# Optimization experiments

Measured on AMD Instinct MI355X. Metric: run time of the kernel, lower is better.

## Reference

```python
import jax, jax.numpy as jnp
import numpy as np

N, E, D, H, G = 50000, 1_600_000, 13, 32, 128
EPS = 1e-5


def _lin(k, fan_in, fan_out):
    kw, kb = jax.random.split(k)
    bound = 1.0 / np.sqrt(fan_in)
    W = jax.random.uniform(kw, (fan_in, fan_out), jnp.float32, -bound, bound)
    b = jax.random.uniform(kb, (fan_out,), jnp.float32, -bound, bound)
    return W, b


def setup_inputs() -> dict:
    key = jax.random.key(0)
    ks = jax.random.split(key, 10)
    x = jax.random.normal(ks[0], (N, D), jnp.float32)
    edge_index = jax.random.randint(ks[1], (2, E), 0, N)
    batch = jnp.sort(jax.random.randint(ks[2], (N,), 0, G))
    bn_gamma = jnp.ones((D,), jnp.float32)
    bn_beta = jnp.zeros((D,), jnp.float32)
    in_w1, in_b1 = _lin(ks[3], D, H)
    in_w2, in_b2 = _lin(ks[4], H, H)
    conv_w1, conv_b1 = _lin(ks[5], 2 * (H + D), 2 * H)
    conv_w2, conv_b2 = _lin(ks[6], 2 * H, H)
    out_w1, out_b1 = _lin(ks[7], H + D, H)
    out_w2, out_b2 = _lin(ks[8], H, 1)
    return dict(x=x, edge_index=edge_index, batch=batch,
                bn_gamma=bn_gamma, bn_beta=bn_beta,
                in_w1=in_w1, in_b1=in_b1, in_w2=in_w2, in_b2=in_b2,
                conv_w1=conv_w1, conv_b1=conv_b1, conv_w2=conv_w2, conv_b2=conv_b2,
                out_w1=out_w1, out_b1=out_b1, out_w2=out_w2, out_b2=out_b2)


def reference(x, edge_index, batch, bn_gamma, bn_beta,
              in_w1, in_b1, in_w2, in_b2,
              conv_w1, conv_b1, conv_w2, conv_b2,
              out_w1, out_b1, out_w2, out_b2):
    # BatchNorm1d (training-mode batch statistics, biased variance)
    mu = jnp.mean(x, axis=0)
    var = jnp.mean((x - mu) ** 2, axis=0)
    X = (x - mu) / jnp.sqrt(var + EPS) * bn_gamma + bn_beta  # [N, D]
    # inputnet
    Hn = jnp.tanh(jax.nn.relu(X @ in_w1 + in_b1) @ in_w2 + in_b2)  # [N, H]
    feat = jnp.concatenate([Hn, X], axis=-1)  # [N, H+D]
    # n_iters = 1 EdgeConv iteration: message = nn([x_i, x_j - x_i]), aggr='add' at target i
    src, dst = edge_index[0], edge_index[1]
    x_i = feat[dst]                               # [E, H+D] target
    x_j = feat[src]                               # [E, H+D] source
    m = jnp.concatenate([x_i, x_j - x_i], axis=-1)  # [E, 2(H+D)]
    m = jnp.tanh(jax.nn.relu(m @ conv_w1 + conv_b1) @ conv_w2 + conv_b2)  # [E, H]
    Hn = jax.ops.segment_sum(m, dst, num_segments=N)  # [N, H]
    feat = jnp.concatenate([Hn, X], axis=-1)  # [N, H+D]
    # global_mean_pool over graphs
    sums = jax.ops.segment_sum(feat, batch, num_segments=G)  # [G, H+D]
    counts = jax.ops.segment_sum(jnp.ones((feat.shape[0], 1), feat.dtype), batch, num_segments=G)
    x_mean = sums / jnp.maximum(counts, 1.0)
    # outputnet
    return jax.nn.sigmoid(jax.nn.relu(x_mean @ out_w1 + out_b1) @ out_w2 + out_b2)  # [G, 1]
```

## Files before the change

### kernel.cpp

```cpp
#include <hip/hip_runtime.h>


typedef __attribute__((ext_vector_type(4))) float floatx4;
typedef __attribute__((ext_vector_type(8))) short short8;
typedef __attribute__((ext_vector_type(8))) _Float16 half8;
typedef __attribute__((ext_vector_type(2))) __fp16 fp16x2;

__device__ __forceinline__ unsigned short f2bf(float f) {
    unsigned int u = __float_as_uint(f);
    u += 0x7FFFu + ((u >> 16) & 1u);
    return (unsigned short)(u >> 16);
}
__device__ __forceinline__ unsigned short f2h(float f) {
    _Float16 h = (_Float16)f;
    return __builtin_bit_cast(unsigned short, h);
}
__device__ __forceinline__ float h2f(unsigned short u) {
    return (float)__builtin_bit_cast(_Float16, u);
}
__device__ __forceinline__ float fast_tanh(float x) {
    float ax = fminf(fabsf(x), 20.0f);
    float e = __expf(2.0f * ax);
    float r = 1.0f - 2.0f * __builtin_amdgcn_rcpf(e + 1.0f);
    return copysignf(r, x);
}
__device__ __forceinline__ float fast_sigmoid(float x) {
    float xc = fminf(fmaxf(x, -30.f), 30.f);
    return 1.0f / (1.0f + __expf(-xc));
}
__device__ __forceinline__ unsigned int pk_h2(float a, float b) {
    fp16x2 p = __builtin_amdgcn_cvt_pkrtz(a, b);
    return __builtin_bit_cast(unsigned int, p);
}
__device__ __forceinline__ void atomic_pk_add_f16(unsigned short* addr, unsigned int packed) {
    asm volatile("global_atomic_pk_add_f16 %0, %1, off" :: "v"(addr), "v"(packed) : "memory");
}

#define NBLK_STAT 120

__global__ __launch_bounds__(256) void k_bnstat(const float* __restrict__ x, int N,
                                                float* __restrict__ part,
                                                uint4* __restrict__ HnZ, int hnq,
                                                float* __restrict__ gacc, int gn) {
    int tid = blockIdx.x * blockDim.x + threadIdx.x;
    int stride = gridDim.x * blockDim.x;
    uint4 z4 = make_uint4(0u, 0u, 0u, 0u);
    for (int i = tid; i < hnq; i += stride) HnZ[i] = z4;
    for (int i = tid; i < gn; i += stride) gacc[i] = 0.f;

    float s[13], q[13];
#pragma unroll
    for (int d = 0; d < 13; d++) { s[d] = 0.f; q[d] = 0.f; }
    for (int n = tid; n < N; n += stride) {
        const float* row = x + (size_t)n * 13;
#pragma unroll
        for (int d = 0; d < 13; d++) { float f = row[d]; s[d] += f; q[d] += f * f; }
    }
#pragma unroll
    for (int d = 0; d < 13; d++) {
        for (int off = 32; off > 0; off >>= 1) {
            s[d] += __shfl_down(s[d], off, 64);
            q[d] += __shfl_down(q[d], off, 64);
        }
    }
    __shared__ float red[4][26];
    int w = threadIdx.x >> 6;
    if ((threadIdx.x & 63) == 0) {
#pragma unroll
        for (int d = 0; d < 13; d++) { red[w][d] = s[d]; red[w][13 + d] = q[d]; }
    }
    __syncthreads();
    if (threadIdx.x < 26) {
        float v = red[0][threadIdx.x] + red[1][threadIdx.x] + red[2][threadIdx.x] + red[3][threadIdx.x];
        int d = threadIdx.x;
        if (d < 13) part[blockIdx.x * 32 + d] = v;
        else        part[NBLK_STAT * 32 + blockIdx.x * 32 + (d - 13)] = v;
    }
}

#define FP 72
#define WP 72
__global__ __launch_bounds__(128) void k_node(
    const float* __restrict__ x, const int* __restrict__ batch,
    const float* __restrict__ bn_g, const float* __restrict__ bn_b,
    const float* __restrict__ in_w1, const float* __restrict__ in_b1,
    const float* __restrict__ in_w2, const float* __restrict__ in_b2,
    const float* __restrict__ conv_w1, const float* __restrict__ conv_b1,
    const float* __restrict__ part,
    unsigned short* __restrict__ A, unsigned short* __restrict__ Bm,
    float* __restrict__ gacc, int N) {
    __shared__ float sW1[13 * 32], sB1[32], sW2[32 * 32], sB2[32];
    __shared__ float sScl[16], sShf[16];
    __shared__ unsigned short sWcatT[128 * WP];
    __shared__ unsigned short sFeat[128 * FP];
    int tid = threadIdx.x;

    for (int i = tid; i < 13 * 32; i += 128) sW1[i] = in_w1[i];
    if (tid < 32) { sB1[tid] = in_b1[tid]; sB2[tid] = in_b2[tid]; }
    for (int i = tid; i < 32 * 32; i += 128) sW2[i] = in_w2[i];
    for (int i = tid; i < 128 * 64; i += 128) {
        int c = i >> 6, k = i & 63;
        float v = 0.f;
        if (k < 45) {
            int cc = c & 63;
            float bot = conv_w1[(45 + k) * 64 + cc];
            v = (c < 64) ? (conv_w1[k * 64 + cc] - bot) : bot;
        }
        sWcatT[c * WP + k] = f2bf(v);
    }
    if (tid < 13) {
        float su = 0.f, sq = 0.f;
        for (int b = 0; b < NBLK_STAT; b++) {
            su += part[b * 32 + tid];
            sq += part[NBLK_STAT * 32 + b * 32 + tid];
        }
        float invN = 1.0f / (float)N;
        float mu = su * invN;
        float var = fmaxf(sq * invN - mu * mu, 0.f);
        float sc = bn_g[tid] / sqrtf(var + 1e-5f);
        sScl[tid] = sc;
        sShf[tid] = bn_b[tid] - mu * sc;
    }
    __syncthreads();

    int n = blockIdx.x * 128 + tid;
    bool valid = (n < N);
    int nl = valid ? n : (N - 1);

    float X[13];
#pragma unroll
    for (int d = 0; d < 13; d++)
        X[d] = x[(size_t)nl * 13 + d] * sScl[d] + sShf[d];
    float h1[32];
#pragma unroll
    for (int j = 0; j < 32; j++) {
        float acc = sB1[j];
#pragma unroll
        for (int d = 0; d < 13; d++) acc += X[d] * sW1[d * 32 + j];
        h1[j] = fmaxf(acc, 0.f);
    }
    float h2[32];
#pragma unroll
    for (int j = 0; j < 32; j++) {
        float acc = sB2[j];
#pragma unroll
        for (int k = 0; k < 32; k++) acc += h1[k] * sW2[k * 32 + j];
        h2[j] = fast_tanh(acc);
    }

    unsigned int fw[16];
#pragma unroll
    for (int i = 0; i < 16; i++) fw[i] = 0;
    if (valid) {
#pragma unroll
        for (int i = 0; i < 16; i++)
            fw[i] = (unsigned)f2bf(h2[2 * i]) | ((unsigned)f2bf(h2[2 * i + 1]) << 16);
    }
    unsigned int xw[7];
#pragma unroll
    for (int i = 0; i < 7; i++) xw[i] = 0;
    if (valid) {
#pragma unroll
        for (int i = 0; i < 6; i++)
            xw[i] = (unsigned)f2bf(X[2 * i]) | ((unsigned)f2bf(X[2 * i + 1]) << 16);
        xw[6] = (unsigned)f2bf(X[12]);
    }
    {
        unsigned short* row = sFeat + tid * FP;
        ((uint4*)row)[0] = make_uint4(fw[0], fw[1], fw[2], fw[3]);
        ((uint4*)row)[1] = make_uint4(fw[4], fw[5], fw[6], fw[7]);
        ((uint4*)row)[2] = make_uint4(fw[8], fw[9], fw[10], fw[11]);
        ((uint4*)row)[3] = make_uint4(fw[12], fw[13], fw[14], fw[15]);
        ((uint4*)row)[4] = make_uint4(xw[0], xw[1], xw[2], xw[3]);
        ((uint4*)row)[5] = make_uint4(xw[4], xw[5], xw[6], 0u);
        ((uint4*)row)[6] = make_uint4(0u, 0u, 0u, 0u);
        ((uint4*)row)[7] = make_uint4(0u, 0u, 0u, 0u);
    }

    {
        int g = valid ? batch[n] : -1;
        unsigned long long uni = __ballot(g == __shfl(g, 0, 64));
        if (uni == ~0ull && g >= 0) {
            float red[14];
#pragma unroll
            for (int d = 0; d < 13; d++) red[d] = X[d];
            red[13] = 1.0f;
#pragma unroll
            for (int d = 0; d < 14; d++)
                for (int off = 32; off > 0; off >>= 1)
                    red[d] += __shfl_down(red[d], off, 64);
            if ((tid & 63) == 0) {
#pragma unroll
                for (int d = 0; d < 13; d++) unsafeAtomicAdd(&gacc[g * 46 + 32 + d], red[d]);
                unsafeAtomicAdd(&gacc[g * 46 + 45], red[13]);
            }
        } else if (valid) {
#pragma unroll
            for (int d = 0; d < 13; d++) unsafeAtomicAdd(&gacc[g * 46 + 32 + d], X[d]);
            unsafeAtomicAdd(&gacc[g * 46 + 45], 1.0f);
        }
    }
    __syncthreads();

    int lane = tid & 63;
    int w = tid >> 6;
    int q = lane >> 4;
    int m = lane & 15;

    short8 wf[2][8];
#pragma unroll
    for (int ks = 0; ks < 2; ks++)
#pragma unroll
        for (int t = 0; t < 8; t++) {
            wf[ks][t] = *(const short8*)(sWcatT + (t * 16 + m) * WP + ks * 32 + q * 8);
        }
    float cb1v[4];
#pragma unroll
    for (int t = 0; t < 4; t++) cb1v[t] = conv_b1[t * 16 + m];

    int base = blockIdx.x * 128 + w * 64;
#pragma unroll
    for (int tile = 0; tile < 4; tile++) {
        const unsigned short* ar = sFeat + (w * 64 + tile * 16 + m) * FP;
        short8 a0 = *(const short8*)(ar + q * 8);
        short8 a1 = *(const short8*)(ar + 32 + q * 8);
        floatx4 c[8];
#pragma unroll
        for (int t = 0; t < 8; t++) {
            floatx4 z = {0.f, 0.f, 0.f, 0.f};
            c[t] = __builtin_amdgcn_mfma_f32_16x16x32_bf16(a0, wf[0][t], z, 0, 0, 0);
            c[t] = __builtin_amdgcn_mfma_f32_16x16x32_bf16(a1, wf[1][t], c[t], 0, 0, 0);
        }
#pragma unroll
        for (int r = 0; r < 4; r++) {
            int row = base + tile * 16 + (q << 2) + r;
            if (row < N) {
#pragma unroll
                for (int t = 0; t < 4; t++)
                    A[(size_t)row * 64 + t * 16 + m] = f2h(c[t][r] + cb1v[t]);
#pragma unroll
                for (int t = 4; t < 8; t++)
                    Bm[(size_t)row * 64 + (t - 4) * 16 + m] = f2h(c[t][r]);
            }
        }
    }
}

__global__ __launch_bounds__(256) void k_edge(
    const int* __restrict__ ei,
    const unsigned short* __restrict__ A, const unsigned short* __restrict__ Bm,
    const float* __restrict__ conv_w2, const float* __restrict__ conv_b2,
    unsigned short* __restrict__ Hn, int E) {
    int lane = threadIdx.x & 63;
    int wid  = blockIdx.x * (blockDim.x >> 6) + (threadIdx.x >> 6);
    int nw   = gridDim.x * (blockDim.x >> 6);
    int q = lane >> 4;
    int m = lane & 15;

    half8 wf[2][2];
#pragma unroll
    for (int s = 0; s < 2; s++)
#pragma unroll
        for (int t = 0; t < 2; t++)
#pragma unroll
            for (int j = 0; j < 8; j++)
                wf[s][t][j] = (_Float16)conv_w2[(s * 32 + q * 8 + j) * 32 + 2 * m + t];
    float cb2a = conv_b2[2 * m];
    float cb2b = conv_b2[2 * m + 1];

    const int* srcp = ei;
    const int* dstp = ei + E;
    int npairs = E >> 5;

    const half8 zero8 = (half8)(_Float16)0.0f;

    for (int p = wid; p < npairs; p += nw) {
        int e0 = p << 5;
        int vd0 = dstp[e0 + m];
        int vs0 = srcp[e0 + m];
        int vd1 = dstp[e0 + 16 + m];
        int vs1 = srcp[e0 + 16 + m];
        uint4 av0a = *(const uint4*)(A  + (size_t)vd0 * 64 + q * 8);
        uint4 av0b = *(const uint4*)(A  + (size_t)vd0 * 64 + 32 + q * 8);
        uint4 bv0a = *(const uint4*)(Bm + (size_t)vs0 * 64 + q * 8);
        uint4 bv0b = *(const uint4*)(Bm + (size_t)vs0 * 64 + 32 + q * 8);
        uint4 av1a = *(const uint4*)(A  + (size_t)vd1 * 64 + q * 8);
        uint4 av1b = *(const uint4*)(A  + (size_t)vd1 * 64 + 32 + q * 8);
        uint4 bv1a = *(const uint4*)(Bm + (size_t)vs1 * 64 + q * 8);
        uint4 bv1b = *(const uint4*)(Bm + (size_t)vs1 * 64 + 32 + q * 8);

        floatx4 c00 = {0.f, 0.f, 0.f, 0.f}, c01 = {0.f, 0.f, 0.f, 0.f};
        floatx4 c10 = {0.f, 0.f, 0.f, 0.f}, c11 = {0.f, 0.f, 0.f, 0.f};

        auto mk = [&zero8](uint4 av, uint4 bv) -> half8 {
            half8 a = __builtin_bit_cast(half8, av);
            half8 b = __builtin_bit_cast(half8, bv);
            half8 s = a + b;
            return __builtin_elementwise_max(s, zero8);
        };
        half8 h0a = mk(av0a, bv0a);
        half8 h0b = mk(av0b, bv0b);
        half8 h1a = mk(av1a, bv1a);
        half8 h1b = mk(av1b, bv1b);

        c00 = __builtin_amdgcn_mfma_f32_16x16x32_f16(h0a, wf[0][0], c00, 0, 0, 0);
        c01 = __builtin_amdgcn_mfma_f32_16x16x32_f16(h0a, wf[0][1], c01, 0, 0, 0);
        c10 = __builtin_amdgcn_mfma_f32_16x16x32_f16(h1a, wf[0][0], c10, 0, 0, 0);
        c11 = __builtin_amdgcn_mfma_f32_16x16x32_f16(h1a, wf[0][1], c11, 0, 0, 0);
        c00 = __builtin_amdgcn_mfma_f32_16x16x32_f16(h0b, wf[1][0], c00, 0, 0, 0);
        c01 = __builtin_amdgcn_mfma_f32_16x16x32_f16(h0b, wf[1][1], c01, 0, 0, 0);
        c10 = __builtin_amdgcn_mfma_f32_16x16x32_f16(h1b, wf[1][0], c10, 0, 0, 0);
        c11 = __builtin_amdgcn_mfma_f32_16x16x32_f16(h1b, wf[1][1], c11, 0, 0, 0);

#pragma unroll
        for (int r = 0; r < 4; r++) {
            int m2 = (q << 2) + r;
            int dd0 = __shfl(vd0, m2, 64);
            int dd1 = __shfl(vd1, m2, 64);
            float o00 = fast_tanh(c00[r] + cb2a);
            float o01 = fast_tanh(c01[r] + cb2b);
            float o10 = fast_tanh(c10[r] + cb2a);
            float o11 = fast_tanh(c11[r] + cb2b);
            atomic_pk_add_f16(Hn + (size_t)dd0 * 32 + 2 * m, pk_h2(o00, o01));
            atomic_pk_add_f16(Hn + (size_t)dd1 * 32 + 2 * m, pk_h2(o10, o11));
        }
    }

    int tstart = npairs << 5;
    int tail = E - tstart;
    if (tail && wid == 0 && lane < tail) {
        int e = tstart + lane;
        int vd = dstp[e], vs = srcp[e];
        float h[64];
        for (int k = 0; k < 64; k++) {
            float a = h2f(A[(size_t)vd * 64 + k]);
            float b = h2f(Bm[(size_t)vs * 64 + k]);
            h[k] = fmaxf(a + b, 0.f);
        }
        for (int j = 0; j < 16; j++) {
            float acc0 = conv_b2[2 * j], acc1 = conv_b2[2 * j + 1];
            for (int k = 0; k < 64; k++) {
                acc0 += h[k] * conv_w2[k * 32 + 2 * j];
                acc1 += h[k] * conv_w2[k * 32 + 2 * j + 1];
            }
            atomic_pk_add_f16(Hn + (size_t)vd * 32 + 2 * j, pk_h2(fast_tanh(acc0), fast_tanh(acc1)));
        }
    }
}

__global__ __launch_bounds__(256) void k_pool(const unsigned short* __restrict__ Hn,
                                              const int* __restrict__ batch,
                                              float* __restrict__ gacc, int N) {
    const int NPB = 512;
    int c = threadIdx.x & 31;
    int r = threadIdx.x >> 5;
    int n0 = blockIdx.x * NPB;
    int nend = min(n0 + NPB, N);
    int gcur = -1;
    float acc = 0.f;
    for (int n = n0 + r; n < nend; n += 8) {
        int g = batch[n];
        if (g != gcur) {
            if (gcur >= 0) unsafeAtomicAdd(&gacc[gcur * 46 + c], acc);
            gcur = g; acc = 0.f;
        }
        acc += h2f(Hn[(size_t)n * 32 + c]);
    }
    if (gcur >= 0) unsafeAtomicAdd(&gacc[gcur * 46 + c], acc);
}

__global__ void k_out(const float* __restrict__ gacc,
                      const float* __restrict__ out_w1, const float* __restrict__ out_b1,
                      const float* __restrict__ out_w2, const float* __restrict__ out_b2,
                      float* __restrict__ out, int G) {
    int g = blockIdx.x * blockDim.x + threadIdx.x;
    if (g >= G) return;
    float cnt = fmaxf(gacc[g * 46 + 45], 1.0f);
    float inv = 1.0f / cnt;
    float f[45];
#pragma unroll
    for (int i = 0; i < 45; i++) f[i] = gacc[g * 46 + i] * inv;
    float h[32];
#pragma unroll
    for (int j = 0; j < 32; j++) {
        float acc = out_b1[j];
#pragma unroll
        for (int k = 0; k < 45; k++) acc += f[k] * out_w1[k * 32 + j];
        h[j] = fmaxf(acc, 0.f);
    }
    float o = out_b2[0];
#pragma unroll
    for (int j = 0; j < 32; j++) o += h[j] * out_w2[j];
    out[g] = fast_sigmoid(o);
}

extern "C" void kernel_launch(void* const* d_in, const int* in_sizes, int n_in,
                              void* d_out, int out_size, void* d_ws, size_t ws_size,
                              hipStream_t stream) {
    const float* x      = (const float*)d_in[0];
    const int*   ei     = (const int*)d_in[1];
    const int*   batch  = (const int*)d_in[2];
    const float* bn_g   = (const float*)d_in[3];
    const float* bn_b   = (const float*)d_in[4];
    const float* in_w1  = (const float*)d_in[5];
    const float* in_b1  = (const float*)d_in[6];
    const float* in_w2  = (const float*)d_in[7];
    const float* in_b2  = (const float*)d_in[8];
    const float* cw1    = (const float*)d_in[9];
    const float* cb1    = (const float*)d_in[10];
    const float* cw2    = (const float*)d_in[11];
    const float* cb2    = (const float*)d_in[12];
    const float* ow1    = (const float*)d_in[13];
    const float* ob1    = (const float*)d_in[14];
    const float* ow2    = (const float*)d_in[15];
    const float* ob2    = (const float*)d_in[16];

    int N = in_sizes[0] / 13;
    int E = in_sizes[1] / 2;
    int G = out_size;
    int Npad = (N + 255) & ~255;

    auto al = [](size_t v) { return (v + 255) & ~(size_t)255; };
    char* ws = (char*)d_ws;
    size_t hn_off   = 0;
    size_t gacc_off = al((size_t)N * 32 * 2);
    size_t part_off = gacc_off + al((size_t)G * 46 * 4);
    size_t a_off    = part_off + al(2 * NBLK_STAT * 32 * 4);
    size_t b_off    = a_off + al((size_t)Npad * 64 * 2);

    unsigned short* Hn = (unsigned short*)(ws + hn_off);
    float* gacc = (float*)(ws + gacc_off);
    float* part = (float*)(ws + part_off);
    unsigned short* A  = (unsigned short*)(ws + a_off);
    unsigned short* Bm = (unsigned short*)(ws + b_off);

    int hnq = (N * 32 * 2) / 16;
    int gn  = G * 46;

    k_bnstat<<<NBLK_STAT, 256, 0, stream>>>(x, N, part, (uint4*)Hn, hnq, gacc, gn);
    k_node<<<(N + 127) / 128, 128, 0, stream>>>(x, batch, bn_g, bn_b,
                                                in_w1, in_b1, in_w2, in_b2,
                                                cw1, cb1, part, A, Bm, gacc, N);
    k_edge<<<2048, 256, 0, stream>>>(ei, A, Bm, cw2, cb2, Hn, E);
    k_pool<<<(N + 511) / 512, 256, 0, stream>>>(Hn, batch, gacc, N);
    k_out<<<1, 128, 0, stream>>>(gacc, ow1, ob1, ow2, ob2, (float*)d_out, G);
}
```

Before: 285.9 us.

## Build CSR by destination and replace atomic edge scatter with per-node gather

```diff
diff --git a/kernel.cpp b/kernel.cpp
--- a/kernel.cpp
+++ b/kernel.cpp
@@ -32,21 +32,17 @@
     fp16x2 p = __builtin_amdgcn_cvt_pkrtz(a, b);
     return __builtin_bit_cast(unsigned int, p);
 }
-__device__ __forceinline__ void atomic_pk_add_f16(unsigned short* addr, unsigned int packed) {
-    asm volatile("global_atomic_pk_add_f16 %0, %1, off" :: "v"(addr), "v"(packed) : "memory");
-}
 
 #define NBLK_STAT 120
 
 __global__ __launch_bounds__(256) void k_bnstat(const float* __restrict__ x, int N,
                                                 float* __restrict__ part,
-                                                uint4* __restrict__ HnZ, int hnq,
-                                                float* __restrict__ gacc, int gn) {
+                                                float* __restrict__ gacc, int gn,
+                                                int* __restrict__ cnt, int cn) {
     int tid = blockIdx.x * blockDim.x + threadIdx.x;
     int stride = gridDim.x * blockDim.x;
-    uint4 z4 = make_uint4(0u, 0u, 0u, 0u);
-    for (int i = tid; i < hnq; i += stride) HnZ[i] = z4;
     for (int i = tid; i < gn; i += stride) gacc[i] = 0.f;
+    for (int i = tid; i < cn; i += stride) cnt[i] = 0;
 
     float s[13], q[13];
 #pragma unroll
@@ -75,6 +71,68 @@
         int d = threadIdx.x;
         if (d < 13) part[blockIdx.x * 32 + d] = v;
         else        part[NBLK_STAT * 32 + blockIdx.x * 32 + (d - 13)] = v;
+    }
+}
+
+__global__ __launch_bounds__(256) void k_hist(const int* __restrict__ ei,
+                                              int* __restrict__ cnt, int E) {
+    const int* dstp = ei + E;
+    int tid = blockIdx.x * blockDim.x + threadIdx.x;
+    int stride = gridDim.x * blockDim.x;
+    for (int e = tid; e < E; e += stride) atomicAdd(&cnt[dstp[e]], 1);
+}
+
+__global__ __launch_bounds__(1024) void k_scan1(int* __restrict__ cnt,
+                                                int* __restrict__ bsum, int N) {
+    __shared__ int sd[1024];
+    int t = threadIdx.x;
+    int i = blockIdx.x * 1024 + t;
+    int v = (i < N) ? cnt[i] : 0;
+    sd[t] = v;
+    __syncthreads();
+    for (int off = 1; off < 1024; off <<= 1) {
+        int a = (t >= off) ? sd[t - off] : 0;
+        __syncthreads();
+        sd[t] += a;
+        __syncthreads();
+    }
+    if (i < N) cnt[i] = sd[t] - v;
+    if (t == 1023) bsum[blockIdx.x] = sd[1023];
+}
+
+__global__ __launch_bounds__(256) void k_fill(const int* __restrict__ cnt,
+                                              const int* __restrict__ bsum,
+                                              int* __restrict__ cursor, int N, int nb) {
+    __shared__ int sboff[64];
+    int t = threadIdx.x;
+    if (t < 64) {
+        int v = (t < nb) ? bsum[t] : 0;
+        for (int off = 1; off < 64; off <<= 1) {
+            int u = __shfl_up(v, off, 64);
+            if (t >= off) v += u;
+        }
+        sboff[t] = v;
+    }
+    __syncthreads();
+    int i = blockIdx.x * blockDim.x + t;
+    if (i < N) {
+        int blk = i >> 10;
+        int boff = (blk == 0) ? 0 : sboff[blk - 1];
+        cursor[i] = cnt[i] + boff;
+    }
+}
+
+__global__ __launch_bounds__(256) void k_scatter(const int* __restrict__ ei,
+                                                 int* __restrict__ cursor,
+                                                 int* __restrict__ ssorted, int E) {
+    const int* srcp = ei;
+    const int* dstp = ei + E;
+    int tid = blockIdx.x * blockDim.x + threadIdx.x;
+    int stride = gridDim.x * blockDim.x;
+    for (int e = tid; e < E; e += stride) {
+        int d = dstp[e];
+        int pos = atomicAdd(&cursor[d], 1);
+        ssorted[pos] = srcp[e];
     }
 }
 
@@ -246,11 +304,12 @@
     }
 }
 
-__global__ __launch_bounds__(256) void k_edge(
-    const int* __restrict__ ei,
+__global__ __launch_bounds__(256) void k_edge2(
+    const int* __restrict__ cursor,
+    const int* __restrict__ ssorted,
     const unsigned short* __restrict__ A, const unsigned short* __restrict__ Bm,
     const float* __restrict__ conv_w2, const float* __restrict__ conv_b2,
-    unsigned short* __restrict__ Hn, int E) {
+    unsigned short* __restrict__ Hn, int N) {
     int lane = threadIdx.x & 63;
     int wid  = blockIdx.x * (blockDim.x >> 6) + (threadIdx.x >> 6);
     int nw   = gridDim.x * (blockDim.x >> 6);
@@ -268,83 +327,64 @@
     float cb2a = conv_b2[2 * m];
     float cb2b = conv_b2[2 * m + 1];
 
-    const int* srcp = ei;
-    const int* dstp = ei + E;
-    int npairs = E >> 5;
-
     const half8 zero8 = (half8)(_Float16)0.0f;
 
-    for (int p = wid; p < npairs; p += nw) {
-        int e0 = p << 5;
-        int vd0 = dstp[e0 + m];
-        int vs0 = srcp[e0 + m];
-        int vd1 = dstp[e0 + 16 + m];
-        int vs1 = srcp[e0 + 16 + m];
-        uint4 av0a = *(const uint4*)(A  + (size_t)vd0 * 64 + q * 8);
-        uint4 av0b = *(const uint4*)(A  + (size_t)vd0 * 64 + 32 + q * 8);
-        uint4 bv0a = *(const uint4*)(Bm + (size_t)vs0 * 64 + q * 8);
-        uint4 bv0b = *(const uint4*)(Bm + (size_t)vs0 * 64 + 32 + q * 8);
-        uint4 av1a = *(const uint4*)(A  + (size_t)vd1 * 64 + q * 8);
-        uint4 av1b = *(const uint4*)(A  + (size_t)vd1 * 64 + 32 + q * 8);
-        uint4 bv1a = *(const uint4*)(Bm + (size_t)vs1 * 64 + q * 8);
-        uint4 bv1b = *(const uint4*)(Bm + (size_t)vs1 * 64 + 32 + q * 8);
-
-        floatx4 c00 = {0.f, 0.f, 0.f, 0.f}, c01 = {0.f, 0.f, 0.f, 0.f};
-        floatx4 c10 = {0.f, 0.f, 0.f, 0.f}, c11 = {0.f, 0.f, 0.f, 0.f};
-
-        auto mk = [&zero8](uint4 av, uint4 bv) -> half8 {
-            half8 a = __builtin_bit_cast(half8, av);
-            half8 b = __builtin_bit_cast(half8, bv);
-            half8 s = a + b;
-            return __builtin_elementwise_max(s, zero8);
-        };
-        half8 h0a = mk(av0a, bv0a);
-        half8 h0b = mk(av0b, bv0b);
-        half8 h1a = mk(av1a, bv1a);
-        half8 h1b = mk(av1b, bv1b);
-
-        c00 = __builtin_amdgcn_mfma_f32_16x16x32_f16(h0a, wf[0][0], c00, 0, 0, 0);
-        c01 = __builtin_amdgcn_mfma_f32_16x16x32_f16(h0a, wf[0][1], c01, 0, 0, 0);
-        c10 = __builtin_amdgcn_mfma_f32_16x16x32_f16(h1a, wf[0][0], c10, 0, 0, 0);
-        c11 = __builtin_amdgcn_mfma_f32_16x16x32_f16(h1a, wf[0][1], c11, 0, 0, 0);
-        c00 = __builtin_amdgcn_mfma_f32_16x16x32_f16(h0b, wf[1][0], c00, 0, 0, 0);
-        c01 = __builtin_amdgcn_mfma_f32_16x16x32_f16(h0b, wf[1][1], c01, 0, 0, 0);
-        c10 = __builtin_amdgcn_mfma_f32_16x16x32_f16(h1b, wf[1][0], c10, 0, 0, 0);
-        c11 = __builtin_amdgcn_mfma_f32_16x16x32_f16(h1b, wf[1][1], c11, 0, 0, 0);
-
-#pragma unroll
-        for (int r = 0; r < 4; r++) {
-            int m2 = (q << 2) + r;
-            int dd0 = __shfl(vd0, m2, 64);
-            int dd1 = __shfl(vd1, m2, 64);
-            float o00 = fast_tanh(c00[r] + cb2a);
-            float o01 = fast_tanh(c01[r] + cb2b);
-            float o10 = fast_tanh(c10[r] + cb2a);
-            float o11 = fast_tanh(c11[r] + cb2b);
-            atomic_pk_add_f16(Hn + (size_t)dd0 * 32 + 2 * m, pk_h2(o00, o01));
-            atomic_pk_add_f16(Hn + (size_t)dd1 * 32 + 2 * m, pk_h2(o10, o11));
-        }
-    }
-
-    int tstart = npairs << 5;
-    int tail = E - tstart;
-    if (tail && wid == 0 && lane < tail) {
-        int e = tstart + lane;
-        int vd = dstp[e], vs = srcp[e];
-        float h[64];
-        for (int k = 0; k < 64; k++) {
-            float a = h2f(A[(size_t)vd * 64 + k]);
-            float b = h2f(Bm[(size_t)vs * 64 + k]);
-            h[k] = fmaxf(a + b, 0.f);
-        }
-        for (int j = 0; j < 16; j++) {
-            float acc0 = conv_b2[2 * j], acc1 = conv_b2[2 * j + 1];
-            for (int k = 0; k < 64; k++) {
-                acc0 += h[k] * conv_w2[k * 32 + 2 * j];
-                acc1 += h[k] * conv_w2[k * 32 + 2 * j + 1];
+    for (int d = wid; d < N; d += nw) {
+        int end = cursor[d];
+        int beg = (d == 0) ? 0 : cursor[d - 1];
+        int deg = end - beg;
+
+        half8 af0 = __builtin_bit_cast(half8, *(const uint4*)(A + (size_t)d * 64 + q * 8));
+        half8 af1 = __builtin_bit_cast(half8, *(const uint4*)(A + (size_t)d * 64 + 32 + q * 8));
+
+        float acc0 = 0.f, acc1 = 0.f;
+        for (int c = 0; c < deg; c += 32) {
+            int lim = end - 1;
+            int i0 = beg + c + m;
+            int s0 = ssorted[min(i0, lim)];
+            int s1 = ssorted[min(i0 + 16, lim)];
+            uint4 b0a = *(const uint4*)(Bm + (size_t)s0 * 64 + q * 8);
+            uint4 b0b = *(const uint4*)(Bm + (size_t)s0 * 64 + 32 + q * 8);
+            uint4 b1a = *(const uint4*)(Bm + (size_t)s1 * 64 + q * 8);
+            uint4 b1b = *(const uint4*)(Bm + (size_t)s1 * 64 + 32 + q * 8);
+
+            half8 h0a = __builtin_elementwise_max(af0 + __builtin_bit_cast(half8, b0a), zero8);
+            half8 h0b = __builtin_elementwise_max(af1 + __builtin_bit_cast(half8, b0b), zero8);
+            half8 h1a = __builtin_elementwise_max(af0 + __builtin_bit_cast(half8, b1a), zero8);
+            half8 h1b = __builtin_elementwise_max(af1 + __builtin_bit_cast(half8, b1b), zero8);
+
+            floatx4 c00 = {0.f, 0.f, 0.f, 0.f}, c01 = {0.f, 0.f, 0.f, 0.f};
+            floatx4 c10 = {0.f, 0.f, 0.f, 0.f}, c11 = {0.f, 0.f, 0.f, 0.f};
+            c00 = __builtin_amdgcn_mfma_f32_16x16x32_f16(h0a, wf[0][0], c00, 0, 0, 0);
+            c01 = __builtin_amdgcn_mfma_f32_16x16x32_f16(h0a, wf[0][1], c01, 0, 0, 0);
+            c10 = __builtin_amdgcn_mfma_f32_16x16x32_f16(h1a, wf[0][0], c10, 0, 0, 0);
+            c11 = __builtin_amdgcn_mfma_f32_16x16x32_f16(h1a, wf[0][1], c11, 0, 0, 0);
+            c00 = __builtin_amdgcn_mfma_f32_16x16x32_f16(h0b, wf[1][0], c00, 0, 0, 0);
+            c01 = __builtin_amdgcn_mfma_f32_16x16x32_f16(h0b, wf[1][1], c01, 0, 0, 0);
+            c10 = __builtin_amdgcn_mfma_f32_16x16x32_f16(h1b, wf[1][0], c10, 0, 0, 0);
+            c11 = __builtin_amdgcn_mfma_f32_16x16x32_f16(h1b, wf[1][1], c11, 0, 0, 0);
+
+            int j = q << 2;
+#pragma unroll
+            for (int r = 0; r < 4; r++) {
+                bool v0 = (c + j + r) < deg;
+                bool v1 = (c + 16 + j + r) < deg;
+                float t00 = fast_tanh(c00[r] + cb2a);
+                float t01 = fast_tanh(c01[r] + cb2b);
+                float t10 = fast_tanh(c10[r] + cb2a);
+                float t11 = fast_tanh(c11[r] + cb2b);
+                acc0 += v0 ? t00 : 0.f;
+                acc1 += v0 ? t01 : 0.f;
+                acc0 += v1 ? t10 : 0.f;
+                acc1 += v1 ? t11 : 0.f;
             }
-            atomic_pk_add_f16(Hn + (size_t)vd * 32 + 2 * j, pk_h2(fast_tanh(acc0), fast_tanh(acc1)));
-        }
+        }
+        acc0 += __shfl_xor(acc0, 16, 64);
+        acc0 += __shfl_xor(acc0, 32, 64);
+        acc1 += __shfl_xor(acc1, 16, 64);
+        acc1 += __shfl_xor(acc1, 32, 64);
+        if (q == 0)
+            *(unsigned int*)(Hn + (size_t)d * 32 + 2 * m) = pk_h2(acc0, acc1);
     }
 }
 
@@ -427,21 +467,33 @@
     size_t part_off = gacc_off + al((size_t)G * 46 * 4);
     size_t a_off    = part_off + al(2 * NBLK_STAT * 32 * 4);
     size_t b_off    = a_off + al((size_t)Npad * 64 * 2);
+    size_t cnt_off  = b_off + al((size_t)Npad * 64 * 2);
+    size_t bsum_off = cnt_off + al((size_t)N * 4);
+    size_t cur_off  = bsum_off + al(64 * 4);
+    size_t srt_off  = cur_off + al((size_t)N * 4);
 
     unsigned short* Hn = (unsigned short*)(ws + hn_off);
     float* gacc = (float*)(ws + gacc_off);
     float* part = (float*)(ws + part_off);
     unsigned short* A  = (unsigned short*)(ws + a_off);
     unsigned short* Bm = (unsigned short*)(ws + b_off);
-
-    int hnq = (N * 32 * 2) / 16;
+    int* cnt     = (int*)(ws + cnt_off);
+    int* bsum    = (int*)(ws + bsum_off);
+    int* cursor  = (int*)(ws + cur_off);
+    int* ssorted = (int*)(ws + srt_off);
+
     int gn  = G * 46;
-
-    k_bnstat<<<NBLK_STAT, 256, 0, stream>>>(x, N, part, (uint4*)Hn, hnq, gacc, gn);
+    int nb1 = (N + 1023) >> 10;
+
+    k_bnstat<<<NBLK_STAT, 256, 0, stream>>>(x, N, part, gacc, gn, cnt, N);
+    k_hist<<<512, 256, 0, stream>>>(ei, cnt, E);
+    k_scan1<<<nb1, 1024, 0, stream>>>(cnt, bsum, N);
+    k_fill<<<(N + 255) / 256, 256, 0, stream>>>(cnt, bsum, cursor, N, nb1);
+    k_scatter<<<1024, 256, 0, stream>>>(ei, cursor, ssorted, E);
     k_node<<<(N + 127) / 128, 128, 0, stream>>>(x, batch, bn_g, bn_b,
                                                 in_w1, in_b1, in_w2, in_b2,
                                                 cw1, cb1, part, A, Bm, gacc, N);
-    k_edge<<<2048, 256, 0, stream>>>(ei, A, Bm, cw2, cb2, Hn, E);
+    k_edge2<<<2048, 256, 0, stream>>>(cursor, ssorted, A, Bm, cw2, cb2, Hn, N);
     k_pool<<<(N + 511) / 512, 256, 0, stream>>>(Hn, batch, gacc, N);
     k_out<<<1, 128, 0, stream>>>(gacc, ow1, ob1, ow2, ob2, (float*)d_out, G);
 }
```

Measured after the change: 464.0 us. +62.3%, slower.

## Fuse edge, pool and output kernels into one cooperative kernel with grid syncs

Applied to the files above, without the earlier changes.

```diff
diff --git a/kernel.cpp b/kernel.cpp
--- a/kernel.cpp
+++ b/kernel.cpp
@@ -1,10 +1,13 @@
 #include <hip/hip_runtime.h>
+#include <hip/hip_cooperative_groups.h>
 
 
 typedef __attribute__((ext_vector_type(4))) float floatx4;
 typedef __attribute__((ext_vector_type(8))) short short8;
 typedef __attribute__((ext_vector_type(8))) _Float16 half8;
 typedef __attribute__((ext_vector_type(2))) __fp16 fp16x2;
+
+namespace cg = cooperative_groups;
 
 __device__ __forceinline__ unsigned short f2bf(float f) {
     unsigned int u = __float_as_uint(f);
@@ -91,6 +94,7 @@
     float* __restrict__ gacc, int N) {
     __shared__ float sW1[13 * 32], sB1[32], sW2[32 * 32], sB2[32];
     __shared__ float sScl[16], sShf[16];
+    __shared__ float sRedS[13][8], sRedQ[13][8];
     __shared__ unsigned short sWcatT[128 * WP];
     __shared__ unsigned short sFeat[128 * FP];
     int tid = threadIdx.x;
@@ -108,12 +112,20 @@
         }
         sWcatT[c * WP + k] = f2bf(v);
     }
+    if (tid < 104) {
+        int d = tid >> 3, j = tid & 7;
+        float su = 0.f, sq = 0.f;
+        for (int b = j; b < NBLK_STAT; b += 8) {
+            su += part[b * 32 + d];
+            sq += part[NBLK_STAT * 32 + b * 32 + d];
+        }
+        sRedS[d][j] = su; sRedQ[d][j] = sq;
+    }
+    __syncthreads();
     if (tid < 13) {
         float su = 0.f, sq = 0.f;
-        for (int b = 0; b < NBLK_STAT; b++) {
-            su += part[b * 32 + tid];
-            sq += part[NBLK_STAT * 32 + b * 32 + tid];
-        }
+#pragma unroll
+        for (int j = 0; j < 8; j++) { su += sRedS[tid][j]; sq += sRedQ[tid][j]; }
         float invN = 1.0f / (float)N;
         float mu = su * invN;
         float var = fmaxf(sq * invN - mu * mu, 0.f);
@@ -246,152 +258,164 @@
     }
 }
 
-__global__ __launch_bounds__(256) void k_edge(
+__global__ __launch_bounds__(256, 4) void k_fused(
     const int* __restrict__ ei,
     const unsigned short* __restrict__ A, const unsigned short* __restrict__ Bm,
     const float* __restrict__ conv_w2, const float* __restrict__ conv_b2,
-    unsigned short* __restrict__ Hn, int E) {
-    int lane = threadIdx.x & 63;
-    int wid  = blockIdx.x * (blockDim.x >> 6) + (threadIdx.x >> 6);
-    int nw   = gridDim.x * (blockDim.x >> 6);
-    int q = lane >> 4;
-    int m = lane & 15;
-
-    half8 wf[2][2];
-#pragma unroll
-    for (int s = 0; s < 2; s++)
-#pragma unroll
-        for (int t = 0; t < 2; t++)
-#pragma unroll
-            for (int j = 0; j < 8; j++)
-                wf[s][t][j] = (_Float16)conv_w2[(s * 32 + q * 8 + j) * 32 + 2 * m + t];
-    float cb2a = conv_b2[2 * m];
-    float cb2b = conv_b2[2 * m + 1];
-
-    const int* srcp = ei;
-    const int* dstp = ei + E;
-    int npairs = E >> 5;
-
-    const half8 zero8 = (half8)(_Float16)0.0f;
-
-    for (int p = wid; p < npairs; p += nw) {
-        int e0 = p << 5;
-        int vd0 = dstp[e0 + m];
-        int vs0 = srcp[e0 + m];
-        int vd1 = dstp[e0 + 16 + m];
-        int vs1 = srcp[e0 + 16 + m];
-        uint4 av0a = *(const uint4*)(A  + (size_t)vd0 * 64 + q * 8);
-        uint4 av0b = *(const uint4*)(A  + (size_t)vd0 * 64 + 32 + q * 8);
-        uint4 bv0a = *(const uint4*)(Bm + (size_t)vs0 * 64 + q * 8);
-        uint4 bv0b = *(const uint4*)(Bm + (size_t)vs0 * 64 + 32 + q * 8);
-        uint4 av1a = *(const uint4*)(A  + (size_t)vd1 * 64 + q * 8);
-        uint4 av1b = *(const uint4*)(A  + (size_t)vd1 * 64 + 32 + q * 8);
-        uint4 bv1a = *(const uint4*)(Bm + (size_t)vs1 * 64 + q * 8);
-        uint4 bv1b = *(const uint4*)(Bm + (size_t)vs1 * 64 + 32 + q * 8);
-
-        floatx4 c00 = {0.f, 0.f, 0.f, 0.f}, c01 = {0.f, 0.f, 0.f, 0.f};
-        floatx4 c10 = {0.f, 0.f, 0.f, 0.f}, c11 = {0.f, 0.f, 0.f, 0.f};
-
-        auto mk = [&zero8](uint4 av, uint4 bv) -> half8 {
-            half8 a = __builtin_bit_cast(half8, av);
-            half8 b = __builtin_bit_cast(half8, bv);
-            half8 s = a + b;
-            return __builtin_elementwise_max(s, zero8);
-        };
-        half8 h0a = mk(av0a, bv0a);
-        half8 h0b = mk(av0b, bv0b);
-        half8 h1a = mk(av1a, bv1a);
-        half8 h1b = mk(av1b, bv1b);
-
-        c00 = __builtin_amdgcn_mfma_f32_16x16x32_f16(h0a, wf[0][0], c00, 0, 0, 0);
-        c01 = __builtin_amdgcn_mfma_f32_16x16x32_f16(h0a, wf[0][1], c01, 0, 0, 0);
-        c10 = __builtin_amdgcn_mfma_f32_16x16x32_f16(h1a, wf[0][0], c10, 0, 0, 0);
-        c11 = __builtin_amdgcn_mfma_f32_16x16x32_f16(h1a, wf[0][1], c11, 0, 0, 0);
-        c00 = __builtin_amdgcn_mfma_f32_16x16x32_f16(h0b, wf[1][0], c00, 0, 0, 0);
-        c01 = __builtin_amdgcn_mfma_f32_16x16x32_f16(h0b, wf[1][1], c01, 0, 0, 0);
-        c10 = __builtin_amdgcn_mfma_f32_16x16x32_f16(h1b, wf[1][0], c10, 0, 0, 0);
-        c11 = __builtin_amdgcn_mfma_f32_16x16x32_f16(h1b, wf[1][1], c11, 0, 0, 0);
-
-#pragma unroll
-        for (int r = 0; r < 4; r++) {
-            int m2 = (q << 2) + r;
-            int dd0 = __shfl(vd0, m2, 64);
-            int dd1 = __shfl(vd1, m2, 64);
-            float o00 = fast_tanh(c00[r] + cb2a);
-            float o01 = fast_tanh(c01[r] + cb2b);
-            float o10 = fast_tanh(c10[r] + cb2a);
-            float o11 = fast_tanh(c11[r] + cb2b);
-            atomic_pk_add_f16(Hn + (size_t)dd0 * 32 + 2 * m, pk_h2(o00, o01));
-            atomic_pk_add_f16(Hn + (size_t)dd1 * 32 + 2 * m, pk_h2(o10, o11));
-        }
-    }
-
-    int tstart = npairs << 5;
-    int tail = E - tstart;
-    if (tail && wid == 0 && lane < tail) {
-        int e = tstart + lane;
-        int vd = dstp[e], vs = srcp[e];
-        float h[64];
-        for (int k = 0; k < 64; k++) {
-            float a = h2f(A[(size_t)vd * 64 + k]);
-            float b = h2f(Bm[(size_t)vs * 64 + k]);
-            h[k] = fmaxf(a + b, 0.f);
-        }
-        for (int j = 0; j < 16; j++) {
-            float acc0 = conv_b2[2 * j], acc1 = conv_b2[2 * j + 1];
+    unsigned short* __restrict__ Hn,
+    const int* __restrict__ batch, float* __restrict__ gacc,
+    const float* __restrict__ out_w1, const float* __restrict__ out_b1,
+    const float* __restrict__ out_w2, const float* __restrict__ out_b2,
+    float* __restrict__ out, int E, int N, int G) {
+    cg::grid_group grid = cg::this_grid();
+
+    {
+        int lane = threadIdx.x & 63;
+        int wid  = blockIdx.x * 4 + (threadIdx.x >> 6);
+        int nw   = gridDim.x * 4;
+        int q = lane >> 4;
+        int m = lane & 15;
+
+        half8 wf[2][2];
+#pragma unroll
+        for (int s = 0; s < 2; s++)
+#pragma unroll
+            for (int t = 0; t < 2; t++)
+#pragma unroll
+                for (int j = 0; j < 8; j++)
+                    wf[s][t][j] = (_Float16)conv_w2[(s * 32 + q * 8 + j) * 32 + 2 * m + t];
+        float cb2a = conv_b2[2 * m];
+        float cb2b = conv_b2[2 * m + 1];
+
+        const int* srcp = ei;
+        const int* dstp = ei + E;
+        int npairs = E >> 5;
+
+        const half8 zero8 = (half8)(_Float16)0.0f;
+
+        for (int p = wid; p < npairs; p += nw) {
+            int e0 = p << 5;
+            int vd0 = dstp[e0 + m];
+            int vs0 = srcp[e0 + m];
+            int vd1 = dstp[e0 + 16 + m];
+            int vs1 = srcp[e0 + 16 + m];
+            uint4 av0a = *(const uint4*)(A  + (size_t)vd0 * 64 + q * 8);
+            uint4 av0b = *(const uint4*)(A  + (size_t)vd0 * 64 + 32 + q * 8);
+            uint4 bv0a = *(const uint4*)(Bm + (size_t)vs0 * 64 + q * 8);
+            uint4 bv0b = *(const uint4*)(Bm + (size_t)vs0 * 64 + 32 + q * 8);
+            uint4 av1a = *(const uint4*)(A  + (size_t)vd1 * 64 + q * 8);
+            uint4 av1b = *(const uint4*)(A  + (size_t)vd1 * 64 + 32 + q * 8);
+            uint4 bv1a = *(const uint4*)(Bm + (size_t)vs1 * 64 + q * 8);
+            uint4 bv1b = *(const uint4*)(Bm + (size_t)vs1 * 64 + 32 + q * 8);
+
+            auto mk = [&zero8](uint4 av, uint4 bv) -> half8 {
+                half8 a = __builtin_bit_cast(half8, av);
+                half8 b = __builtin_bit_cast(half8, bv);
+                half8 s = a + b;
+                return __builtin_elementwise_max(s, zero8);
+            };
+            half8 h0a = mk(av0a, bv0a);
+            half8 h0b = mk(av0b, bv0b);
+            half8 h1a = mk(av1a, bv1a);
+            half8 h1b = mk(av1b, bv1b);
+
+            floatx4 c00 = {0.f, 0.f, 0.f, 0.f}, c01 = {0.f, 0.f, 0.f, 0.f};
+            floatx4 c10 = {0.f, 0.f, 0.f, 0.f}, c11 = {0.f, 0.f, 0.f, 0.f};
+            c00 = __builtin_amdgcn_mfma_f32_16x16x32_f16(h0a, wf[0][0], c00, 0, 0, 0);
+            c01 = __builtin_amdgcn_mfma_f32_16x16x32_f16(h0a, wf[0][1], c01, 0, 0, 0);
+            c10 = __builtin_amdgcn_mfma_f32_16x16x32_f16(h1a, wf[0][0], c10, 0, 0, 0);
+            c11 = __builtin_amdgcn_mfma_f32_16x16x32_f16(h1a, wf[0][1], c11, 0, 0, 0);
+            c00 = __builtin_amdgcn_mfma_f32_16x16x32_f16(h0b, wf[1][0], c00, 0, 0, 0);
+            c01 = __builtin_amdgcn_mfma_f32_16x16x32_f16(h0b, wf[1][1], c01, 0, 0, 0);
+            c10 = __builtin_amdgcn_mfma_f32_16x16x32_f16(h1b, wf[1][0], c10, 0, 0, 0);
+            c11 = __builtin_amdgcn_mfma_f32_16x16x32_f16(h1b, wf[1][1], c11, 0, 0, 0);
+
+#pragma unroll
+            for (int r = 0; r < 4; r++) {
+                int m2 = (q << 2) + r;
+                int dd0 = __shfl(vd0, m2, 64);
+                int dd1 = __shfl(vd1, m2, 64);
+                float o00 = fast_tanh(c00[r] + cb2a);
+                float o01 = fast_tanh(c01[r] + cb2b);
+                float o10 = fast_tanh(c10[r] + cb2a);
+                float o11 = fast_tanh(c11[r] + cb2b);
+                atomic_pk_add_f16(Hn + (size_t)dd0 * 32 + 2 * m, pk_h2(o00, o01));
+                atomic_pk_add_f16(Hn + (size_t)dd1 * 32 + 2 * m, pk_h2(o10, o11));
+            }
+        }
+
+        int tstart = npairs << 5;
+        int tail = E - tstart;
+        if (tail && wid == 0 && lane < tail) {
+            int e = tstart + lane;
+            int vd = dstp[e], vs = srcp[e];
+            float h[64];
             for (int k = 0; k < 64; k++) {
-                acc0 += h[k] * conv_w2[k * 32 + 2 * j];
-                acc1 += h[k] * conv_w2[k * 32 + 2 * j + 1];
-            }
-            atomic_pk_add_f16(Hn + (size_t)vd * 32 + 2 * j, pk_h2(fast_tanh(acc0), fast_tanh(acc1)));
-        }
-    }
-}
-
-__global__ __launch_bounds__(256) void k_pool(const unsigned short* __restrict__ Hn,
-                                              const int* __restrict__ batch,
-                                              float* __restrict__ gacc, int N) {
-    const int NPB = 512;
-    int c = threadIdx.x & 31;
-    int r = threadIdx.x >> 5;
-    int n0 = blockIdx.x * NPB;
-    int nend = min(n0 + NPB, N);
-    int gcur = -1;
-    float acc = 0.f;
-    for (int n = n0 + r; n < nend; n += 8) {
-        int g = batch[n];
-        if (g != gcur) {
+                float a = h2f(A[(size_t)vd * 64 + k]);
+                float b = h2f(Bm[(size_t)vs * 64 + k]);
+                h[k] = fmaxf(a + b, 0.f);
+            }
+            for (int j = 0; j < 16; j++) {
+                float acc0 = conv_b2[2 * j], acc1 = conv_b2[2 * j + 1];
+                for (int k = 0; k < 64; k++) {
+                    acc0 += h[k] * conv_w2[k * 32 + 2 * j];
+                    acc1 += h[k] * conv_w2[k * 32 + 2 * j + 1];
+                }
+                atomic_pk_add_f16(Hn + (size_t)vd * 32 + 2 * j, pk_h2(fast_tanh(acc0), fast_tanh(acc1)));
+            }
+        }
+    }
+
+    __threadfence();
+    grid.sync();
+
+    {
+        const int NPB = 512;
+        int nchunks = (N + NPB - 1) / NPB;
+        int c = threadIdx.x & 31;
+        int r = threadIdx.x >> 5;
+        for (int chunk = blockIdx.x; chunk < nchunks; chunk += gridDim.x) {
+            int n0 = chunk * NPB;
+            int nend = min(n0 + NPB, N);
+            int gcur = -1;
+            float acc = 0.f;
+            for (int n = n0 + r; n < nend; n += 8) {
+                int g = batch[n];
+                if (g != gcur) {
+                    if (gcur >= 0) unsafeAtomicAdd(&gacc[gcur * 46 + c], acc);
+                    gcur = g; acc = 0.f;
+                }
+                acc += h2f(Hn[(size_t)n * 32 + c]);
+            }
             if (gcur >= 0) unsafeAtomicAdd(&gacc[gcur * 46 + c], acc);
-            gcur = g; acc = 0.f;
-        }
-        acc += h2f(Hn[(size_t)n * 32 + c]);
-    }
-    if (gcur >= 0) unsafeAtomicAdd(&gacc[gcur * 46 + c], acc);
-}
-
-__global__ void k_out(const float* __restrict__ gacc,
-                      const float* __restrict__ out_w1, const float* __restrict__ out_b1,
-                      const float* __restrict__ out_w2, const float* __restrict__ out_b2,
-                      float* __restrict__ out, int G) {
-    int g = blockIdx.x * blockDim.x + threadIdx.x;
-    if (g >= G) return;
-    float cnt = fmaxf(gacc[g * 46 + 45], 1.0f);
-    float inv = 1.0f / cnt;
-    float f[45];
-#pragma unroll
-    for (int i = 0; i < 45; i++) f[i] = gacc[g * 46 + i] * inv;
-    float h[32];
-#pragma unroll
-    for (int j = 0; j < 32; j++) {
-        float acc = out_b1[j];
-#pragma unroll
-        for (int k = 0; k < 45; k++) acc += f[k] * out_w1[k * 32 + j];
-        h[j] = fmaxf(acc, 0.f);
-    }
-    float o = out_b2[0];
-#pragma unroll
-    for (int j = 0; j < 32; j++) o += h[j] * out_w2[j];
-    out[g] = fast_sigmoid(o);
+        }
+    }
+
+    __threadfence();
+    grid.sync();
+
+    if (blockIdx.x == 0) {
+        int g = threadIdx.x;
+        if (g < G) {
+            float cnt = fmaxf(gacc[g * 46 + 45], 1.0f);
+            float inv = 1.0f / cnt;
+            float f[45];
+#pragma unroll
+            for (int i = 0; i < 45; i++) f[i] = gacc[g * 46 + i] * inv;
+            float h[32];
+#pragma unroll
+            for (int j = 0; j < 32; j++) {
+                float acc = out_b1[j];
+#pragma unroll
+                for (int k = 0; k < 45; k++) acc += f[k] * out_w1[k * 32 + j];
+                h[j] = fmaxf(acc, 0.f);
+            }
+            float o = out_b2[0];
+#pragma unroll
+            for (int j = 0; j < 32; j++) o += h[j] * out_w2[j];
+            out[g] = fast_sigmoid(o);
+        }
+    }
 }
 
 extern "C" void kernel_launch(void* const* d_in, const int* in_sizes, int n_in,
@@ -437,11 +461,31 @@
     int hnq = (N * 32 * 2) / 16;
     int gn  = G * 46;
 
+    static int s_grid = 0;
+    if (s_grid == 0) {
+        int perCU = 0;
+        hipError_t err = hipOccupancyMaxActiveBlocksPerMultiprocessor(
+            &perCU, (const void*)k_fused, 256, 0);
+        int dev = 0, cus = 0;
+        hipGetDevice(&dev);
+        hipDeviceGetAttribute(&cus, hipDeviceAttributeMultiprocessorCount, dev);
+        if (err != hipSuccess || perCU <= 0) perCU = 4;
+        if (cus <= 0) cus = 256;
+        long cap = (long)perCU * cus;
+        s_grid = (int)(cap < 1024 ? cap : 1024);
+    }
+
     k_bnstat<<<NBLK_STAT, 256, 0, stream>>>(x, N, part, (uint4*)Hn, hnq, gacc, gn);
     k_node<<<(N + 127) / 128, 128, 0, stream>>>(x, batch, bn_g, bn_b,
                                                 in_w1, in_b1, in_w2, in_b2,
                                                 cw1, cb1, part, A, Bm, gacc, N);
-    k_edge<<<2048, 256, 0, stream>>>(ei, A, Bm, cw2, cb2, Hn, E);
-    k_pool<<<(N + 511) / 512, 256, 0, stream>>>(Hn, batch, gacc, N);
-    k_out<<<1, 128, 0, stream>>>(gacc, ow1, ob1, ow2, ob2, (float*)d_out, G);
-}
+    {
+        float* outp = (float*)d_out;
+        void* fargs[] = { (void*)&ei, (void*)&A, (void*)&Bm, (void*)&cw2, (void*)&cb2,
+                          (void*)&Hn, (void*)&batch, (void*)&gacc,
+                          (void*)&ow1, (void*)&ob1, (void*)&ow2, (void*)&ob2,
+                          (void*)&outp, (void*)&E, (void*)&N, (void*)&G };
+        hipLaunchCooperativeKernel((const void*)k_fused, dim3(s_grid), dim3(256),
+                                   fargs, 0, stream);
+    }
+}
```

Result: slower. 512.2 us (+79.2%).
